# Kernel tuning notes

Measured on AMD Instinct MI355X. Metric: run time of the kernel, lower is better.

Reference implementation:

```python
import jax, jax.numpy as jnp
import numpy as np

N = 100000      # nodes
E = 1600000     # edges
D_IN = 2        # num_node_features (hardcoded in module)
EMB = 64        # embedding_size
HID = 128       # hidden_size
NEG_SLOPE = 0.2 # GATv2 leaky_relu default


def setup_inputs() -> dict:
    key = jax.random.key(0)
    ks = jax.random.split(key, 20)
    s = 0.1
    inp = {
        "x": jax.random.normal(ks[0], (N, D_IN), dtype=jnp.float32),
        "edge_index": jax.random.randint(ks[1], (2, E), 0, N, dtype=jnp.int32),
        "edge_attr": jax.random.normal(ks[2], (E, 1), dtype=jnp.float32),
        "target_node_idx": 12345,
        # conv1 params (in=2 -> out=64, heads=1)
        "Wl1": jax.random.normal(ks[3], (D_IN, EMB), dtype=jnp.float32) * s,
        "bl1": jnp.zeros((EMB,), dtype=jnp.float32),
        "Wr1": jax.random.normal(ks[4], (D_IN, EMB), dtype=jnp.float32) * s,
        "br1": jnp.zeros((EMB,), dtype=jnp.float32),
        "We1": jax.random.normal(ks[5], (1, EMB), dtype=jnp.float32) * s,
        "att1": jax.random.normal(ks[6], (EMB,), dtype=jnp.float32) * s,
        "b1": jnp.zeros((EMB,), dtype=jnp.float32),
        # conv2 params (in=64 -> out=64)
        "Wl2": jax.random.normal(ks[7], (EMB, EMB), dtype=jnp.float32) * s,
        "bl2": jnp.zeros((EMB,), dtype=jnp.float32),
        "Wr2": jax.random.normal(ks[8], (EMB, EMB), dtype=jnp.float32) * s,
        "br2": jnp.zeros((EMB,), dtype=jnp.float32),
        "We2": jax.random.normal(ks[9], (1, EMB), dtype=jnp.float32) * s,
        "att2": jax.random.normal(ks[10], (EMB,), dtype=jnp.float32) * s,
        "b2": jnp.zeros((EMB,), dtype=jnp.float32),
        # final linear head
        "Wf": jax.random.normal(ks[11], (EMB, HID), dtype=jnp.float32) * s,
        "bf": jnp.zeros((HID,), dtype=jnp.float32),
    }
    return inp


def _gatv2_layer(x, src, dst, ea, Wl, bl, Wr, br, We, att, b):
    # GATv2: e_ij = att . leaky_relu(Wl x_j + Wr x_i + We ea_ij); out_i = sum_j softmax_i(e_ij) * (Wl x_j)
    xl = x @ Wl + bl                      # [N, C] (source transform)
    xr = x @ Wr + br                      # [N, C] (target transform)
    ee = ea @ We                          # [E', C]
    e = jax.nn.leaky_relu(xl[src] + xr[dst] + ee, NEG_SLOPE)  # [E', C]
    score = e @ att                       # [E']
    m = jax.ops.segment_max(score, dst, num_segments=N)
    ex = jnp.exp(score - m[dst])
    denom = jax.ops.segment_sum(ex, dst, num_segments=N)
    alpha = ex / denom[dst]               # segment softmax over incoming edges
    out = jax.ops.segment_sum(alpha[:, None] * xl[src], dst, num_segments=N)
    return out + b


def reference(x, edge_index, edge_attr, target_node_idx,
              Wl1, bl1, Wr1, br1, We1, att1, b1,
              Wl2, bl2, Wr2, br2, We2, att2, b2,
              Wf, bf):
    # PyG add_self_loops=True with fill_value='mean' for edge_attr
    loop = jnp.arange(N, dtype=edge_index.dtype)
    src = jnp.concatenate([edge_index[0], loop])
    dst = jnp.concatenate([edge_index[1], loop])
    ea_mean = jnp.mean(edge_attr, axis=0, keepdims=True)          # [1,1]
    ea = jnp.concatenate([edge_attr, jnp.broadcast_to(ea_mean, (N, 1))])

    h = _gatv2_layer(x, src, dst, ea, Wl1, bl1, Wr1, br1, We1, att1, b1)
    h = jax.nn.relu(h)
    h = _gatv2_layer(h, src, dst, ea, Wl2, bl2, Wr2, br2, We2, att2, b2)
    h = jax.nn.relu(h)

    t = h[target_node_idx][None, :]       # [1, EMB]
    return t @ Wf + bf                    # [1, HID]
```

## Files before the change

### kernel.cpp

```cpp
#include <hip/hip_runtime.h>
#include <math.h>

#define CAP2   511
#define CAPS1  512
#define CAP1   65536
#define CAPN   512
#define NBLK   512
#define NGRP   8
#define GRPSZ  (NBLK / NGRP)
#define BMW    4096


__device__ __forceinline__ int aload_i(const int* p) {
    return __hip_atomic_load((int*)p, __ATOMIC_RELAXED, __HIP_MEMORY_SCOPE_AGENT);
}
__device__ __forceinline__ void astore_i(int* p, int v) {
    __hip_atomic_store(p, v, __ATOMIC_RELAXED, __HIP_MEMORY_SCOPE_AGENT);
}
__device__ __forceinline__ float aload_f(const float* p) {
    return __hip_atomic_load((float*)p, __ATOMIC_RELAXED, __HIP_MEMORY_SCOPE_AGENT);
}
__device__ __forceinline__ void astore_f(float* p, float v) {
    __hip_atomic_store(p, v, __ATOMIC_RELAXED, __HIP_MEMORY_SCOPE_AGENT);
}

__device__ __forceinline__ void grid_sync(int* bar, int epoch) {
    __syncthreads();
    if (threadIdx.x == 0) {
        int g = blockIdx.x & (NGRP - 1);
        int prev = __hip_atomic_fetch_add(&bar[32 * g], 1,
                     __ATOMIC_RELAXED, __HIP_MEMORY_SCOPE_AGENT);
        if (prev == (epoch + 1) * GRPSZ - 1) {
            int p2 = __hip_atomic_fetch_add(&bar[256], 1,
                       __ATOMIC_RELAXED, __HIP_MEMORY_SCOPE_AGENT);
            if (p2 == (epoch + 1) * NGRP - 1)
                __hip_atomic_store(&bar[288], epoch + 1,
                    __ATOMIC_RELAXED, __HIP_MEMORY_SCOPE_AGENT);
        }
        while (__hip_atomic_load(&bar[288], __ATOMIC_RELAXED,
                                 __HIP_MEMORY_SCOPE_AGENT) < epoch + 1)
            __builtin_amdgcn_s_sleep(2);
    }
    __syncthreads();
}

__global__ __launch_bounds__(256, 4)
void k_mega(const float* __restrict__ x, const int* __restrict__ ei,
            const float* __restrict__ ea, const int* __restrict__ tptr,
            const float* __restrict__ Wl1, const float* __restrict__ bl1,
            const float* __restrict__ Wr1, const float* __restrict__ br1,
            const float* __restrict__ We1, const float* __restrict__ att1,
            const float* __restrict__ b1,
            const float* __restrict__ Wl2, const float* __restrict__ bl2,
            const float* __restrict__ Wr2, const float* __restrict__ br2,
            const float* __restrict__ We2, const float* __restrict__ att2,
            const float* __restrict__ b2,
            const float* __restrict__ Wf, const float* __restrict__ bf,
            int E,
            int* hdr, int* bar, float* partials,
            int* L2_src, float* L2_ea,
            int* L1_src, int* L1_dst, float* L1_ea,
            float* xl2, float* out) {
    int tid = threadIdx.x, lane = tid & 63, wq = tid >> 6;
    int bid = blockIdx.x;
    int gid = bid * 256 + tid;
    const int gstride = NBLK * 256;

    __shared__ float wsum[4];
    __shared__ int   s1[CAPS1];
    __shared__ int   l2idx[CAP2];
    __shared__ int   esrc[CAPN + 1];
    __shared__ float eea[CAPN + 1];
    __shared__ float xsA[CAPN + 1], xsB[CAPN + 1];
    __shared__ float scores[CAPN + 1];
    __shared__ float part[4][64];
    __shared__ float hrow[64];
    __shared__ float xr2s[64];
    __shared__ int   bitmap[BMW];
    __shared__ float m_sh, d_sh, eam_sh;
    __shared__ int   n_sh, scnt;

    {
        int t = tptr[0];
        float local = 0.f;
        const int4*   dst4 = (const int4*)(ei + E);
        const float4* ea4  = (const float4*)ea;
        int E4 = E >> 2;
        for (int e4 = gid; e4 < E4; e4 += gstride) {
            int4 d = dst4[e4];
            float4 a = ea4[e4];
            local += a.x + a.y + a.z + a.w;
            int eb = e4 * 4;
            if (d.x == t) { int p = atomicAdd(&hdr[0], 1); if (p < CAP2) { astore_i(&L2_src[p], ei[eb]);     astore_f(&L2_ea[p], a.x); } }
            if (d.y == t) { int p = atomicAdd(&hdr[0], 1); if (p < CAP2) { astore_i(&L2_src[p], ei[eb + 1]); astore_f(&L2_ea[p], a.y); } }
            if (d.z == t) { int p = atomicAdd(&hdr[0], 1); if (p < CAP2) { astore_i(&L2_src[p], ei[eb + 2]); astore_f(&L2_ea[p], a.z); } }
            if (d.w == t) { int p = atomicAdd(&hdr[0], 1); if (p < CAP2) { astore_i(&L2_src[p], ei[eb + 3]); astore_f(&L2_ea[p], a.w); } }
        }
        if (gid == 0) {
            for (int e = (E >> 2) * 4; e < E; e++) {
                float a = ea[e];
                local += a;
                if (ei[E + e] == t) { int p = atomicAdd(&hdr[0], 1); if (p < CAP2) { astore_i(&L2_src[p], ei[e]); astore_f(&L2_ea[p], a); } }
            }
        }
        for (int o = 32; o >= 1; o >>= 1) local += __shfl_xor(local, o, 64);
        if (lane == 0) wsum[wq] = local;
        __syncthreads();
        if (tid == 0) astore_f(&partials[bid], wsum[0] + wsum[1] + wsum[2] + wsum[3]);
    }
    grid_sync(bar, 0);

    int c2 = aload_i(&hdr[0]); if (c2 > CAP2) c2 = CAP2;
    {
        float local = aload_f(&partials[tid]) + aload_f(&partials[tid + 256]);
        for (int o = 32; o >= 1; o >>= 1) local += __shfl_xor(local, o, 64);
        if (lane == 0) wsum[wq] = local;
        __syncthreads();
        if (tid == 0) eam_sh = (wsum[0] + wsum[1] + wsum[2] + wsum[3]) / (float)E;

        if (wq == 0) {
            int t = tptr[0];
            if (c2 <= 64) {
                int v = (lane < c2) ? aload_i(&L2_src[lane]) : -1;
                int first = lane;
                #pragma unroll
                for (int j = 0; j < 64; j++) {
                    int vj = __shfl(v, j);
                    if (j < first && vj == v) first = j;
                }
                bool isfirst = (lane < c2) && (first == lane) && (v != t);
                unsigned long long bf = __ballot(isfirst);
                int myidx = (v == t) ? 0
                            : (1 + (int)__popcll(bf & ((1ull << lane) - 1)));
                int idx = __shfl(myidx, first);
                if (lane < c2) l2idx[lane] = idx;
                if (isfirst) s1[myidx] = v;
                if (lane == 0) { s1[0] = t; n_sh = 1 + (int)__popcll(bf); }
            } else if (lane == 0) {
                s1[0] = t;
                int n = 1;
                for (int k = 0; k < c2; k++) {
                    int v = aload_i(&L2_src[k]);
                    int idx = -1;
                    for (int j = 0; j < n; j++) if (s1[j] == v) { idx = j; break; }
                    if (idx < 0) { idx = n; s1[n] = v; n++; }
                    l2idx[k] = idx;
                }
                n_sh = n;
            }
        }
        for (int w = tid; w < BMW; w += 256) bitmap[w] = 0;
        __syncthreads();
        int n_s1 = n_sh;
        for (int j = tid; j < n_s1; j += 256) {
            int u = s1[j];
            atomicOr(&bitmap[(u >> 5) & (BMW - 1)], 1 << (u & 31));
        }
        __syncthreads();

        const int4* dst4 = (const int4*)(ei + E);
        int E4 = E >> 2;
        for (int e4 = gid; e4 < E4; e4 += gstride) {
            int4 d = dst4[e4];
            int eb = e4 * 4;
            int dd[4] = {d.x, d.y, d.z, d.w};
            #pragma unroll
            for (int q = 0; q < 4; q++) {
                int dv = dd[q];
                if (bitmap[(dv >> 5) & (BMW - 1)] & (1 << (dv & 31))) {
                    int idx = -1;
                    for (int j = 0; j < n_s1; j++) if (s1[j] == dv) { idx = j; break; }
                    if (idx >= 0) {
                        int p = atomicAdd(&hdr[8], 1);
                        if (p < CAP1) { astore_i(&L1_src[p], ei[eb + q]); astore_i(&L1_dst[p], idx); astore_f(&L1_ea[p], ea[eb + q]); }
                    }
                }
            }
        }
        if (gid == 0) {
            for (int e = E4 * 4; e < E; e++) {
                int dv = ei[E + e];
                int idx = -1;
                for (int j = 0; j < n_s1; j++) if (s1[j] == dv) { idx = j; break; }
                if (idx >= 0) {
                    int p = atomicAdd(&hdr[8], 1);
                    if (p < CAP1) { astore_i(&L1_src[p], ei[e]); astore_i(&L1_dst[p], idx); astore_f(&L1_ea[p], ea[e]); }
                }
            }
        }
    }
    grid_sync(bar, 1);

    int n_s1 = n_sh;
    float eam = eam_sh;

    for (int node = bid; node < n_s1; node += NBLK) {
        int v = s1[node];
        if (tid == 0) scnt = 0;
        __syncthreads();

        int c1 = aload_i(&hdr[8]); if (c1 > CAP1) c1 = CAP1;
        for (int k = tid; k < c1; k += 256) {
            if (aload_i(&L1_dst[k]) == node) {
                int p = atomicAdd(&scnt, 1);
                if (p < CAPN) { esrc[p] = aload_i(&L1_src[k]); eea[p] = aload_f(&L1_ea[k]); }
            }
        }
        __syncthreads();
        int nE = scnt; if (nE > CAPN) nE = CAPN;
        if (tid == 0) { esrc[nE] = v; eea[nE] = eam; }
        __syncthreads();
        nE += 1;

        const float2* x2 = (const float2*)x;
        for (int j = tid; j < nE; j += 256) {
            float2 xv = x2[esrc[j]];
            xsA[j] = xv.x; xsB[j] = xv.y;
        }
        __syncthreads();

        float wl0 = Wl1[lane], wl1w = Wl1[64 + lane], bl = bl1[lane];
        float we = We1[lane], at = att1[lane];
        float2 xv = x2[v];
        float xr = xv.x * Wr1[lane] + xv.y * Wr1[64 + lane] + br1[lane];

        for (int k = wq; k < nE; k += 4) {
            float xl = xsA[k] * wl0 + xsB[k] * wl1w + bl;
            float ev = xl + xr + eea[k] * we;
            ev = ev > 0.f ? ev : 0.2f * ev;
            float p = ev * at;
            for (int o = 32; o >= 1; o >>= 1) p += __shfl_xor(p, o, 64);
            if (lane == 0) scores[k] = p;
        }
        __syncthreads();

        if (wq == 0) {
            float m = -3.4e38f;
            for (int k = lane; k < nE; k += 64) m = fmaxf(m, scores[k]);
            for (int o = 32; o >= 1; o >>= 1) m = fmaxf(m, __shfl_xor(m, o, 64));
            float d = 0.f;
            for (int k = lane; k < nE; k += 64) d += expf(scores[k] - m);
            for (int o = 32; o >= 1; o >>= 1) d += __shfl_xor(d, o, 64);
            if (lane == 0) { m_sh = m; d_sh = d; }
        }
        __syncthreads();
        float m = m_sh, dinv = 1.f / d_sh;

        float acc = 0.f;
        for (int k = wq; k < nE; k += 4) {
            float xl = xsA[k] * wl0 + xsB[k] * wl1w + bl;
            acc += expf(scores[k] - m) * dinv * xl;
        }
        part[wq][lane] = acc;
        __syncthreads();
        if (tid < 64) {
            float h = part[0][lane] + part[1][lane] + part[2][lane] + part[3][lane] + b1[lane];
            hrow[lane] = h > 0.f ? h : 0.f;
        }
        __syncthreads();

        float p = 0.f;
        int k0 = 16 * wq;
        for (int k = k0; k < k0 + 16; k++) p += hrow[k] * Wl2[k * 64 + lane];
        part[wq][lane] = p;
        __syncthreads();
        if (tid < 64)
            astore_f(&xl2[node * 64 + lane],
                     part[0][lane] + part[1][lane] + part[2][lane] + part[3][lane] + bl2[lane]);

        if (node == 0) {
            __syncthreads();
            float p2 = 0.f;
            for (int k = k0; k < k0 + 16; k++) p2 += hrow[k] * Wr2[k * 64 + lane];
            part[wq][lane] = p2;
            __syncthreads();
            if (tid < 64)
                xr2s[lane] = part[0][lane] + part[1][lane] + part[2][lane] + part[3][lane] + br2[lane];
        }
        __syncthreads();
    }
    grid_sync(bar, 2);

    if (bid == 0) {
        int nE2 = c2;
        float* xl2sh = (float*)bitmap;
        int rows = n_s1 < 64 ? n_s1 : 64;
        for (int i = tid; i < rows * 64; i += 256) xl2sh[i] = aload_f(&xl2[i]);
        for (int j = tid; j < nE2; j += 256) eea[j] = aload_f(&L2_ea[j]);
        __syncthreads();

        float we = We2[lane], at = att2[lane], xr = xr2s[lane];
        for (int j = wq; j <= nE2; j += 4) {
            int   idx = (j < nE2) ? l2idx[j] : 0;
            float eav = (j < nE2) ? eea[j]   : eam;
            float xlv = (idx < 64) ? xl2sh[idx * 64 + lane]
                                   : aload_f(&xl2[idx * 64 + lane]);
            float ev = xlv + xr + eav * we;
            ev = ev > 0.f ? ev : 0.2f * ev;
            float p = ev * at;
            for (int o = 32; o >= 1; o >>= 1) p += __shfl_xor(p, o, 64);
            if (lane == 0) scores[j] = p;
        }
        __syncthreads();

        if (wq == 0) {
            int tot = nE2 + 1;
            float m = -3.4e38f;
            for (int j = lane; j < tot; j += 64) m = fmaxf(m, scores[j]);
            for (int o = 32; o >= 1; o >>= 1) m = fmaxf(m, __shfl_xor(m, o, 64));
            float d = 0.f;
            for (int j = lane; j < tot; j += 64) d += expf(scores[j] - m);
            for (int o = 32; o >= 1; o >>= 1) d += __shfl_xor(d, o, 64);
            if (lane == 0) { m_sh = m; d_sh = d; }
        }
        __syncthreads();
        float m = m_sh, dinv = 1.f / d_sh;

        float acc = 0.f;
        for (int j = wq; j <= nE2; j += 4) {
            int idx = (j < nE2) ? l2idx[j] : 0;
            float xlv = (idx < 64) ? xl2sh[idx * 64 + lane]
                                   : aload_f(&xl2[idx * 64 + lane]);
            acc += expf(scores[j] - m) * dinv * xlv;
        }
        part[wq][lane] = acc;
        __syncthreads();
        if (tid < 64) {
            float h = part[0][lane] + part[1][lane] + part[2][lane] + part[3][lane] + b2[lane];
            hrow[lane] = h > 0.f ? h : 0.f;
        }
        __syncthreads();
        if (tid < 128) {
            float r = bf[tid];
            for (int c = 0; c < 64; c++) r += hrow[c] * Wf[c * 128 + tid];
            out[tid] = r;
        }
    }
}

extern "C" void kernel_launch(void* const* d_in, const int* in_sizes, int n_in,
                              void* d_out, int out_size, void* d_ws, size_t ws_size,
                              hipStream_t stream) {
    const float* x    = (const float*)d_in[0];
    const int*   ei   = (const int*)  d_in[1];
    const float* ea   = (const float*)d_in[2];
    const int*   tptr = (const int*)  d_in[3];
    const float* Wl1  = (const float*)d_in[4];
    const float* bl1  = (const float*)d_in[5];
    const float* Wr1  = (const float*)d_in[6];
    const float* br1  = (const float*)d_in[7];
    const float* We1  = (const float*)d_in[8];
    const float* att1 = (const float*)d_in[9];
    const float* b1   = (const float*)d_in[10];
    const float* Wl2  = (const float*)d_in[11];
    const float* bl2  = (const float*)d_in[12];
    const float* Wr2  = (const float*)d_in[13];
    const float* br2  = (const float*)d_in[14];
    const float* We2  = (const float*)d_in[15];
    const float* att2 = (const float*)d_in[16];
    const float* b2   = (const float*)d_in[17];
    const float* Wf   = (const float*)d_in[18];
    const float* bf   = (const float*)d_in[19];

    int E = in_sizes[2];

    char* base = (char*)d_ws;
    int*   hdr      = (int*)base;   base += 256;
    int*   bar      = (int*)base;   base += 1792;
    float* partials = (float*)base; base += NBLK * sizeof(float);
    int*   L2_src   = (int*)base;   base += CAP2 * sizeof(int);
    float* L2_ea    = (float*)base; base += CAP2 * sizeof(float);
    int*   L1_src   = (int*)base;   base += CAP1 * sizeof(int);
    int*   L1_dst   = (int*)base;   base += CAP1 * sizeof(int);
    float* L1_ea    = (float*)base; base += CAP1 * sizeof(float);
    float* xl2      = (float*)base; base += (size_t)CAPS1 * 64 * sizeof(float);

    hipMemsetAsync(hdr, 0, 2048, stream);

    hipLaunchKernelGGL(k_mega, dim3(NBLK), dim3(256), 0, stream,
                       x, ei, ea, tptr,
                       Wl1, bl1, Wr1, br1, We1, att1, b1,
                       Wl2, bl2, Wr2, br2, We2, att2, b2,
                       Wf, bf, E,
                       hdr, bar, partials,
                       L2_src, L2_ea,
                       L1_src, L1_dst, L1_ea,
                       xl2, (float*)d_out);
}
```

Before: 132.6 us.

## Bucket layer-1 edges per node, cache edge chunks in registers, flatten grid barrier

Replaces the flat global L1 edge list, which every node block had to rescan and filter, with per-node buckets filled through per-node atomic counters and packed 64-bit (src, ea) entries. Each block then reads only its own node's edges. The first pass also keeps its destination and edge-attribute chunks in registers so the second pass can reuse them instead of reloading from global memory. The two-level grid barrier becomes 64 leaf counters that block 0 polls with a wave reduction. The costs are higher register pressure, a larger workspace, and a single block acting as the barrier coordinator.

```diff
diff --git a/kernel.cpp b/kernel.cpp
--- a/kernel.cpp
+++ b/kernel.cpp
@@ -3,12 +3,11 @@
 
 #define CAP2   511
 #define CAPS1  512
-#define CAP1   65536
 #define CAPN   512
 #define NBLK   512
-#define NGRP   8
-#define GRPSZ  (NBLK / NGRP)
+#define NLEAF  64
 #define BMW    4096
+#define MAXIT  4
 
 
 __device__ __forceinline__ int aload_i(const int* p) {
@@ -23,23 +22,37 @@
 __device__ __forceinline__ void astore_f(float* p, float v) {
     __hip_atomic_store(p, v, __ATOMIC_RELAXED, __HIP_MEMORY_SCOPE_AGENT);
 }
+__device__ __forceinline__ unsigned long long aload_u64(const unsigned long long* p) {
+    return __hip_atomic_load((unsigned long long*)p, __ATOMIC_RELAXED, __HIP_MEMORY_SCOPE_AGENT);
+}
+__device__ __forceinline__ void astore_u64(unsigned long long* p, unsigned long long v) {
+    __hip_atomic_store(p, v, __ATOMIC_RELAXED, __HIP_MEMORY_SCOPE_AGENT);
+}
 
 __device__ __forceinline__ void grid_sync(int* bar, int epoch) {
     __syncthreads();
-    if (threadIdx.x == 0) {
-        int g = blockIdx.x & (NGRP - 1);
-        int prev = __hip_atomic_fetch_add(&bar[32 * g], 1,
-                     __ATOMIC_RELAXED, __HIP_MEMORY_SCOPE_AGENT);
-        if (prev == (epoch + 1) * GRPSZ - 1) {
-            int p2 = __hip_atomic_fetch_add(&bar[256], 1,
-                       __ATOMIC_RELAXED, __HIP_MEMORY_SCOPE_AGENT);
-            if (p2 == (epoch + 1) * NGRP - 1)
-                __hip_atomic_store(&bar[288], epoch + 1,
-                    __ATOMIC_RELAXED, __HIP_MEMORY_SCOPE_AGENT);
-        }
-        while (__hip_atomic_load(&bar[288], __ATOMIC_RELAXED,
-                                 __HIP_MEMORY_SCOPE_AGENT) < epoch + 1)
-            __builtin_amdgcn_s_sleep(2);
+    if (threadIdx.x < 64) {
+        int lane = threadIdx.x;
+        if (lane == 0)
+            __hip_atomic_fetch_add(&bar[32 * (blockIdx.x & (NLEAF - 1))], 1,
+                                   __ATOMIC_RELAXED, __HIP_MEMORY_SCOPE_AGENT);
+        if (blockIdx.x == 0) {
+            int target = (epoch + 1) * NBLK;
+            for (;;) {
+                int v = __hip_atomic_load(&bar[32 * lane], __ATOMIC_RELAXED,
+                                          __HIP_MEMORY_SCOPE_AGENT);
+                for (int o = 32; o >= 1; o >>= 1) v += __shfl_xor(v, o, 64);
+                if (v >= target) break;
+                __builtin_amdgcn_s_sleep(1);
+            }
+            if (lane == 0)
+                __hip_atomic_store(&bar[32 * NLEAF], epoch + 1,
+                                   __ATOMIC_RELAXED, __HIP_MEMORY_SCOPE_AGENT);
+        } else if (lane == 0) {
+            while (__hip_atomic_load(&bar[32 * NLEAF], __ATOMIC_RELAXED,
+                                     __HIP_MEMORY_SCOPE_AGENT) < epoch + 1)
+                __builtin_amdgcn_s_sleep(2);
+        }
     }
     __syncthreads();
 }
@@ -57,9 +70,9 @@
             const float* __restrict__ b2,
             const float* __restrict__ Wf, const float* __restrict__ bf,
             int E,
-            int* hdr, int* bar, float* partials,
+            int* hdr, int* bar, int* nodecnt, float* partials,
             int* L2_src, float* L2_ea,
-            int* L1_src, int* L1_dst, float* L1_ea,
+            unsigned long long* buck,
             float* xl2, float* out) {
     int tid = threadIdx.x, lane = tid & 63, wq = tid >> 6;
     int bid = blockIdx.x;
@@ -78,15 +91,38 @@
     __shared__ float xr2s[64];
     __shared__ int   bitmap[BMW];
     __shared__ float m_sh, d_sh, eam_sh;
-    __shared__ int   n_sh, scnt;
-
+    __shared__ int   n_sh;
+
+    const int4*   dst4 = (const int4*)(ei + E);
+    const float4* ea4  = (const float4*)ea;
+    int E4 = E >> 2;
+    int t = tptr[0];
+
+    int4   rc[MAXIT];
+    float4 rea[MAXIT];
+    #pragma unroll
+    for (int i = 0; i < MAXIT; i++) {
+        int e4 = gid + i * gstride;
+        rc[i]  = (e4 < E4) ? dst4[e4] : make_int4(-1, -1, -1, -1);
+        rea[i] = (e4 < E4) ? ea4[e4]  : make_float4(0.f, 0.f, 0.f, 0.f);
+    }
     {
-        int t = tptr[0];
         float local = 0.f;
-        const int4*   dst4 = (const int4*)(ei + E);
-        const float4* ea4  = (const float4*)ea;
-        int E4 = E >> 2;
-        for (int e4 = gid; e4 < E4; e4 += gstride) {
+        #pragma unroll
+        for (int i = 0; i < MAXIT; i++) {
+            int e4 = gid + i * gstride;
+            if (e4 < E4) {
+                float4 a = rea[i];
+                local += a.x + a.y + a.z + a.w;
+                int4 d = rc[i];
+                int eb = e4 * 4;
+                if (d.x == t) { int p = atomicAdd(&hdr[0], 1); if (p < CAP2) { astore_i(&L2_src[p], ei[eb]);     astore_f(&L2_ea[p], a.x); } }
+                if (d.y == t) { int p = atomicAdd(&hdr[0], 1); if (p < CAP2) { astore_i(&L2_src[p], ei[eb + 1]); astore_f(&L2_ea[p], a.y); } }
+                if (d.z == t) { int p = atomicAdd(&hdr[0], 1); if (p < CAP2) { astore_i(&L2_src[p], ei[eb + 2]); astore_f(&L2_ea[p], a.z); } }
+                if (d.w == t) { int p = atomicAdd(&hdr[0], 1); if (p < CAP2) { astore_i(&L2_src[p], ei[eb + 3]); astore_f(&L2_ea[p], a.w); } }
+            }
+        }
+        for (int e4 = gid + MAXIT * gstride; e4 < E4; e4 += gstride) {
             int4 d = dst4[e4];
             float4 a = ea4[e4];
             local += a.x + a.y + a.z + a.w;
@@ -97,7 +133,7 @@
             if (d.w == t) { int p = atomicAdd(&hdr[0], 1); if (p < CAP2) { astore_i(&L2_src[p], ei[eb + 3]); astore_f(&L2_ea[p], a.w); } }
         }
         if (gid == 0) {
-            for (int e = (E >> 2) * 4; e < E; e++) {
+            for (int e = E4 * 4; e < E; e++) {
                 float a = ea[e];
                 local += a;
                 if (ei[E + e] == t) { int p = atomicAdd(&hdr[0], 1); if (p < CAP2) { astore_i(&L2_src[p], ei[e]); astore_f(&L2_ea[p], a); } }
@@ -119,7 +155,6 @@
         if (tid == 0) eam_sh = (wsum[0] + wsum[1] + wsum[2] + wsum[3]) / (float)E;
 
         if (wq == 0) {
-            int t = tptr[0];
             if (c2 <= 64) {
                 int v = (lane < c2) ? aload_i(&L2_src[lane]) : -1;
                 int first = lane;
@@ -129,13 +164,13 @@
                     if (j < first && vj == v) first = j;
                 }
                 bool isfirst = (lane < c2) && (first == lane) && (v != t);
-                unsigned long long bf = __ballot(isfirst);
+                unsigned long long bfm = __ballot(isfirst);
                 int myidx = (v == t) ? 0
-                            : (1 + (int)__popcll(bf & ((1ull << lane) - 1)));
+                            : (1 + (int)__popcll(bfm & ((1ull << lane) - 1)));
                 int idx = __shfl(myidx, first);
                 if (lane < c2) l2idx[lane] = idx;
                 if (isfirst) s1[myidx] = v;
-                if (lane == 0) { s1[0] = t; n_sh = 1 + (int)__popcll(bf); }
+                if (lane == 0) { s1[0] = t; n_sh = 1 + (int)__popcll(bfm); }
             } else if (lane == 0) {
                 s1[0] = t;
                 int n = 1;
@@ -158,9 +193,35 @@
         }
         __syncthreads();
 
-        const int4* dst4 = (const int4*)(ei + E);
-        int E4 = E >> 2;
-        for (int e4 = gid; e4 < E4; e4 += gstride) {
+        #pragma unroll
+        for (int i = 0; i < MAXIT; i++) {
+            int e4 = gid + i * gstride;
+            if (e4 < E4) {
+                int4 d = rc[i];
+                int eb = e4 * 4;
+                int dd[4] = {d.x, d.y, d.z, d.w};
+                float av[4] = {rea[i].x, rea[i].y, rea[i].z, rea[i].w};
+                #pragma unroll
+                for (int q = 0; q < 4; q++) {
+                    int dv = dd[q];
+                    if (dv >= 0 && (bitmap[(dv >> 5) & (BMW - 1)] & (1 << (dv & 31)))) {
+                        int idx = -1;
+                        for (int j = 0; j < n_s1; j++) if (s1[j] == dv) { idx = j; break; }
+                        if (idx >= 0) {
+                            int slot = __hip_atomic_fetch_add(&nodecnt[idx], 1,
+                                         __ATOMIC_RELAXED, __HIP_MEMORY_SCOPE_AGENT);
+                            if (slot < CAPN) {
+                                unsigned long long pk =
+                                    ((unsigned long long)__float_as_uint(av[q]) << 32) |
+                                    (unsigned)ei[eb + q];
+                                astore_u64(&buck[(size_t)idx * CAPN + slot], pk);
+                            }
+                        }
+                    }
+                }
+            }
+        }
+        for (int e4 = gid + MAXIT * gstride; e4 < E4; e4 += gstride) {
             int4 d = dst4[e4];
             int eb = e4 * 4;
             int dd[4] = {d.x, d.y, d.z, d.w};
@@ -171,8 +232,14 @@
                     int idx = -1;
                     for (int j = 0; j < n_s1; j++) if (s1[j] == dv) { idx = j; break; }
                     if (idx >= 0) {
-                        int p = atomicAdd(&hdr[8], 1);
-                        if (p < CAP1) { astore_i(&L1_src[p], ei[eb + q]); astore_i(&L1_dst[p], idx); astore_f(&L1_ea[p], ea[eb + q]); }
+                        int slot = __hip_atomic_fetch_add(&nodecnt[idx], 1,
+                                     __ATOMIC_RELAXED, __HIP_MEMORY_SCOPE_AGENT);
+                        if (slot < CAPN) {
+                            unsigned long long pk =
+                                ((unsigned long long)__float_as_uint(ea[eb + q]) << 32) |
+                                (unsigned)ei[eb + q];
+                            astore_u64(&buck[(size_t)idx * CAPN + slot], pk);
+                        }
                     }
                 }
             }
@@ -183,8 +250,14 @@
                 int idx = -1;
                 for (int j = 0; j < n_s1; j++) if (s1[j] == dv) { idx = j; break; }
                 if (idx >= 0) {
-                    int p = atomicAdd(&hdr[8], 1);
-                    if (p < CAP1) { astore_i(&L1_src[p], ei[e]); astore_i(&L1_dst[p], idx); astore_f(&L1_ea[p], ea[e]); }
+                    int slot = __hip_atomic_fetch_add(&nodecnt[idx], 1,
+                                 __ATOMIC_RELAXED, __HIP_MEMORY_SCOPE_AGENT);
+                    if (slot < CAPN) {
+                        unsigned long long pk =
+                            ((unsigned long long)__float_as_uint(ea[e]) << 32) |
+                            (unsigned)ei[e];
+                        astore_u64(&buck[(size_t)idx * CAPN + slot], pk);
+                    }
                 }
             }
         }
@@ -196,18 +269,14 @@
 
     for (int node = bid; node < n_s1; node += NBLK) {
         int v = s1[node];
-        if (tid == 0) scnt = 0;
-        __syncthreads();
-
-        int c1 = aload_i(&hdr[8]); if (c1 > CAP1) c1 = CAP1;
-        for (int k = tid; k < c1; k += 256) {
-            if (aload_i(&L1_dst[k]) == node) {
-                int p = atomicAdd(&scnt, 1);
-                if (p < CAPN) { esrc[p] = aload_i(&L1_src[k]); eea[p] = aload_f(&L1_ea[k]); }
-            }
-        }
-        __syncthreads();
-        int nE = scnt; if (nE > CAPN) nE = CAPN;
+        int cnt = aload_i(&nodecnt[node]); if (cnt > CAPN) cnt = CAPN;
+        for (int k = tid; k < cnt; k += 256) {
+            unsigned long long pk = aload_u64(&buck[(size_t)node * CAPN + k]);
+            esrc[k] = (int)(unsigned)(pk & 0xffffffffull);
+            eea[k]  = __uint_as_float((unsigned)(pk >> 32));
+        }
+        __syncthreads();
+        int nE = cnt;
         if (tid == 0) { esrc[nE] = v; eea[nE] = eam; }
         __syncthreads();
         nE += 1;
@@ -366,24 +435,23 @@
 
     char* base = (char*)d_ws;
     int*   hdr      = (int*)base;   base += 256;
-    int*   bar      = (int*)base;   base += 1792;
+    int*   bar      = (int*)base;   base += 8448;
+    int*   nodecnt  = (int*)base;   base += 2048;
     float* partials = (float*)base; base += NBLK * sizeof(float);
-    int*   L2_src   = (int*)base;   base += CAP2 * sizeof(int);
-    float* L2_ea    = (float*)base; base += CAP2 * sizeof(float);
-    int*   L1_src   = (int*)base;   base += CAP1 * sizeof(int);
-    int*   L1_dst   = (int*)base;   base += CAP1 * sizeof(int);
-    float* L1_ea    = (float*)base; base += CAP1 * sizeof(float);
+    int*   L2_src   = (int*)base;   base += 512 * sizeof(int);
+    float* L2_ea    = (float*)base; base += 512 * sizeof(float);
+    unsigned long long* buck = (unsigned long long*)base;
+    base += (size_t)CAPS1 * CAPN * sizeof(unsigned long long);
     float* xl2      = (float*)base; base += (size_t)CAPS1 * 64 * sizeof(float);
 
-    hipMemsetAsync(hdr, 0, 2048, stream);
+    hipMemsetAsync(hdr, 0, 256 + 8448 + 2048, stream);
 
     hipLaunchKernelGGL(k_mega, dim3(NBLK), dim3(256), 0, stream,
                        x, ei, ea, tptr,
                        Wl1, bl1, Wr1, br1, We1, att1, b1,
                        Wl2, bl2, Wr2, br2, We2, att2, b2,
                        Wf, bf, E,
-                       hdr, bar, partials,
+                       hdr, bar, nodecnt, partials,
                        L2_src, L2_ea,
-                       L1_src, L1_dst, L1_ea,
-                       xl2, (float*)d_out);
-}
+                       buck, xl2, (float*)d_out);
+}
```

New measurement: 130.8 us. About the same (-1.3%).
